# Kernel optimization log

Measured on AMD Instinct MI355X. Metric: run time of the kernel, lower is better.

## Reference

```python
import jax, jax.numpy as jnp
import numpy as np

B, T, D = 2, 2048, 1024
NUM_HEAD = 8
HEAD_DIM = D // NUM_HEAD
CLIP = 2  # _RELATIVE_POS_CLIP


def setup_inputs() -> dict:
    key = jax.random.key(0)
    ks = jax.random.split(key, 12)
    s = 0.02
    return {
        "query": jax.random.normal(ks[0], (B, T, D), jnp.float32),
        "keys": jax.random.normal(ks[1], (B, T, D), jnp.float32),
        "values": jax.random.normal(ks[2], (B, T, D), jnp.float32),
        "Wq": jax.random.normal(ks[3], (D, D), jnp.float32) * s,
        "bq": jnp.zeros((D,), jnp.float32),
        "Wk": jax.random.normal(ks[4], (D, D), jnp.float32) * s,
        "bk": jnp.zeros((D,), jnp.float32),
        "Wv": jax.random.normal(ks[5], (D, D), jnp.float32) * s,
        "bv": jnp.zeros((D,), jnp.float32),
        "Wo": jax.random.normal(ks[6], (D, D), jnp.float32) * s,
        "bo": jnp.zeros((D,), jnp.float32),
        "relpos_table": jax.random.normal(ks[7], (2 * CLIP + 1, D), jnp.float32) * s,
    }


def reference(query, keys, values, Wq, bq, Wk, bk, Wv, bv, Wo, bo, relpos_table):
    Bq, T2, _ = query.shape
    T1 = keys.shape[1]
    # QKV projections (torch Linear: y = x @ W.T + b)
    tq = query @ Wq.T + bq                      # (B, T2, D)
    tk = keys @ Wk.T + bk                       # (B, T1, D)
    tv = values @ Wv.T + bv                     # (B, T1, D)

    # relative-position logits: relpos_embed[i,j] = table[clip(j-i)+CLIP]
    # faithful math via (B,T2,5) dots + gather instead of (T2,T1,D) broadcast
    relpos = jnp.clip(jnp.arange(T1)[None, :] - jnp.arange(T2)[:, None],
                      -CLIP, CLIP) + CLIP        # (T2, T1) int
    proj = tq @ relpos_table.T                   # (B, T2, 2*CLIP+1)
    relpos_logits = proj[:, jnp.arange(T2)[:, None], relpos]  # (B, T2, T1)

    # split heads
    q = tq.reshape(Bq, T2, NUM_HEAD, HEAD_DIM).transpose(0, 2, 1, 3)
    k = tk.reshape(Bq, T1, NUM_HEAD, HEAD_DIM).transpose(0, 2, 1, 3)
    v = tv.reshape(Bq, T1, NUM_HEAD, HEAD_DIM).transpose(0, 2, 1, 3)

    logits = jnp.einsum("bhqd,bhkd->bhqk", q, k)
    logits = (logits + relpos_logits[:, None]) / jnp.sqrt(
        jnp.asarray(HEAD_DIM, logits.dtype))    # scaling after bias, as in nmtlab
    weights = jax.nn.softmax(logits, axis=-1)   # (B, H, T2, T1)
    ctx = jnp.einsum("bhqk,bhkd->bhqd", weights, v)
    ctx = ctx.transpose(0, 2, 1, 3).reshape(Bq, T2, NUM_HEAD * HEAD_DIM)
    out = ctx @ Wo.T + bo                        # (B, T2, D)
    return out, weights
```

## Files before the change

### kernel.cpp

```cpp
#include <hip/hip_runtime.h>
#include <hip/hip_bf16.h>
#include <cmath>

#define Bsz 2
#define Tsz 2048
#define Dsz 1024
#define Hn  8
#define DH  128
#define SCALE 0.08838834764831845f

typedef __attribute__((ext_vector_type(8))) short short8;
typedef __attribute__((ext_vector_type(4))) short short4v;
typedef __attribute__((ext_vector_type(4))) float f32x4;
typedef __hip_bfloat16 bf16;

#define LDK 136

__device__ __forceinline__ float bf2f(unsigned short u) {
    return __uint_as_float(((unsigned)u) << 16);
}
__device__ __forceinline__ unsigned short f2bf(float f) {
    bf16 h = __float2bfloat16(f);
    return *(unsigned short*)&h;
}
__device__ __forceinline__ short8 pack8(float4 a, float4 b) {
    short8 o;
    o[0] = (short)f2bf(a.x); o[1] = (short)f2bf(a.y);
    o[2] = (short)f2bf(a.z); o[3] = (short)f2bf(a.w);
    o[4] = (short)f2bf(b.x); o[5] = (short)f2bf(b.y);
    o[6] = (short)f2bf(b.z); o[7] = (short)f2bf(b.w);
    return o;
}

__device__ __forceinline__ void gload16(const bf16* g, bf16* l) {
    __builtin_amdgcn_global_load_lds(
        (const __attribute__((address_space(1))) void*)g,
        (__attribute__((address_space(3))) void*)l, 16, 0, 0);
}

struct CvtJob { const float* s; bf16* d; int n; };
struct CvtArgs { CvtJob j[4]; };

__global__ __launch_bounds__(256) void cvt_k(CvtArgs a) {
    CvtJob job = a.j[blockIdx.y];
    int idx = (blockIdx.x * 256 + threadIdx.x) * 8;
    const int stride = gridDim.x * 256 * 8;
    for (; idx < job.n; idx += stride) {
        float4 f0 = *(const float4*)(job.s + idx);
        float4 f1 = *(const float4*)(job.s + idx + 4);
        *(short8*)(job.d + idx) = pack8(f0, f1);
    }
}

__device__ __forceinline__ void mfma_step32(const bf16* As, const bf16* Bs,
                                            f32x4 acc[4][4],
                                            int wr, int wc, int fr, int g)
{
    short8 af[4], bfv[4];
#pragma unroll
    for (int m = 0; m < 4; ++m)
        af[m] = *(const short8*)(As + (wr * 64 + m * 16 + fr) * 32 + g * 8);
#pragma unroll
    for (int n = 0; n < 4; ++n)
        bfv[n] = *(const short8*)(Bs + (wc * 64 + n * 16 + fr) * 32 + g * 8);
#pragma unroll
    for (int m = 0; m < 4; ++m)
#pragma unroll
        for (int n = 0; n < 4; ++n)
            acc[m][n] = __builtin_amdgcn_mfma_f32_16x16x32_bf16(
                af[m], bfv[n], acc[m][n], 0, 0, 0);
}

struct GemmJob { const float* A; const bf16* B; const float* bias; void* C; int mode; };
struct GemmArgs { GemmJob j[3]; };

__global__ __launch_bounds__(256, 3) void gemm_qkv_k(GemmArgs args)
{
    __shared__ __align__(16) bf16 As[128 * 32];
    __shared__ __align__(16) bf16 Bs[128 * 32];
    const int bid = blockIdx.x;
    const int wid = (bid & 7) * 96 + (bid >> 3);
    const GemmJob job = args.j[wid >> 8];
    const int t = wid & 255;
    const int row0 = (t >> 3) * 128;
    const int col0 = (t & 7) * 128;
    const int tid = threadIdx.x;
    const int lane = tid & 63;
    const int w = tid >> 6, wr = w >> 1, wc = w & 1;
    const int fr = lane & 15, g = lane >> 4;

    const int srow = lane >> 2, scol = (lane & 3) * 8;
    const float* Ag0 = job.A + (size_t)(row0 + w * 32 + srow) * Dsz + scol;
    const float* Ag1 = Ag0 + 16 * Dsz;
    const bf16*  Bg  = job.B + (size_t)(col0 + w * 32 + srow) * Dsz + scol;
    const int lofs = __builtin_amdgcn_readfirstlane(w * 1024);
    bf16* Bsw = Bs + lofs;
    bf16* Aw0 = As + lofs + lane * 8;
    bf16* Aw1 = Aw0 + 16 * 32;

    f32x4 acc[4][4];
    const f32x4 vz = {0.f, 0.f, 0.f, 0.f};
#pragma unroll
    for (int m = 0; m < 4; ++m)
#pragma unroll
        for (int n = 0; n < 4; ++n) acc[m][n] = vz;

    float4 fa0 = *(const float4*)(Ag0);
    float4 fa1 = *(const float4*)(Ag0 + 4);
    float4 fa2 = *(const float4*)(Ag1);
    float4 fa3 = *(const float4*)(Ag1 + 4);

#pragma unroll 1
    for (int k0 = 0; k0 < Dsz; k0 += 32) {
        __syncthreads();
        *(short8*)Aw0 = pack8(fa0, fa1);
        *(short8*)Aw1 = pack8(fa2, fa3);
        gload16(Bg + k0, Bsw);
        gload16(Bg + 16 * Dsz + k0, Bsw + 16 * 32);
        __syncthreads();
        if (k0 + 32 < Dsz) {
            fa0 = *(const float4*)(Ag0 + k0 + 32);
            fa1 = *(const float4*)(Ag0 + k0 + 36);
            fa2 = *(const float4*)(Ag1 + k0 + 32);
            fa3 = *(const float4*)(Ag1 + k0 + 36);
        }
        mfma_step32(As, Bs, acc, wr, wc, fr, g);
    }

    if (job.mode == 2) {
        bf16* vtp = (bf16*)job.C;
#pragma unroll
        for (int m = 0; m < 4; ++m) {
            const int gi0 = row0 + wr * 64 + m * 16 + g * 4;
            const int bidx = gi0 >> 11, jj = gi0 & 2047;
#pragma unroll
            for (int n = 0; n < 4; ++n) {
                const int gj = col0 + wc * 64 + n * 16 + fr;
                const float bv = job.bias[gj];
                short4v pk;
#pragma unroll
                for (int r = 0; r < 4; ++r)
                    pk[r] = (short)f2bf(acc[m][n][r] + bv);
                const size_t zrow = ((size_t)bidx * 8 + (gj >> 7)) * 128 + (gj & 127);
                *(short4v*)(vtp + zrow * Tsz + jj) = pk;
            }
        }
    } else {
#pragma unroll
        for (int m = 0; m < 4; ++m) {
#pragma unroll
            for (int r = 0; r < 4; ++r) {
                const int gi = row0 + wr * 64 + m * 16 + g * 4 + r;
#pragma unroll
                for (int n = 0; n < 4; ++n) {
                    const int gj = col0 + wc * 64 + n * 16 + fr;
                    float x = acc[m][n][r] + job.bias[gj];
                    ((bf16*)job.C)[(size_t)gi * Dsz + gj] = __float2bfloat16(x);
                }
            }
        }
    }
}

__global__ __launch_bounds__(256) void relproj_k(
    const bf16* __restrict__ tq, const float* __restrict__ table,
    float* __restrict__ proj)
{
    const int row  = blockIdx.x * 4 + (threadIdx.x >> 6);
    const int lane = threadIdx.x & 63;
    const bf16* qrow = tq + (size_t)row * Dsz;
    float acc[5] = {0.f, 0.f, 0.f, 0.f, 0.f};
#pragma unroll
    for (int t = 0; t < 4; ++t) {
        const int d = t * 256 + lane * 4;
        short4v q4 = *(const short4v*)(qrow + d);
        float qv[4];
#pragma unroll
        for (int q = 0; q < 4; ++q) qv[q] = bf2f((unsigned short)q4[q]);
#pragma unroll
        for (int c = 0; c < 5; ++c) {
            float4 t4 = *(const float4*)(table + c * Dsz + d);
            acc[c] = fmaf(qv[0], t4.x, acc[c]);
            acc[c] = fmaf(qv[1], t4.y, acc[c]);
            acc[c] = fmaf(qv[2], t4.z, acc[c]);
            acc[c] = fmaf(qv[3], t4.w, acc[c]);
        }
    }
#pragma unroll
    for (int c = 0; c < 5; ++c)
        for (int off = 32; off > 0; off >>= 1)
            acc[c] += __shfl_xor(acc[c], off);
    if (lane == 0) {
#pragma unroll
        for (int c = 0; c < 5; ++c)
            proj[(size_t)row * 8 + c] = acc[c];
    }
}

__global__ __launch_bounds__(512) void flash_pv_k(
    const bf16* __restrict__ tq, const bf16* __restrict__ tk,
    const bf16* __restrict__ vt, const float* __restrict__ proj,
    float* __restrict__ invs_g, bf16* __restrict__ ctx)
{
    __shared__ __align__(16) bf16 Ks[128 * LDK];
    __shared__ __align__(16) bf16 Vs[128 * LDK];
    __shared__ __align__(16) bf16 Ps[128 * 128];
    __shared__ float proj_s[5 * 132];

    const int tid = threadIdx.x;
    const int bid = blockIdx.x;
    const int wid = (bid & 7) * 32 + (bid >> 3);
    const int qt = wid & 15, z = wid >> 4;
    const int b = z >> 3, h = z & 7;
    const int i0 = qt * 128;
    const int lane = tid & 63, w = tid >> 6;
    const int fr = lane & 15, g = lane >> 4;
    const int il = w * 16 + fr;
    const int srow = tid >> 2, scb = (tid & 3) * 32;

    if (tid < 128) {
        const float* pr = proj + (size_t)(b * Tsz + i0 + tid) * 8;
#pragma unroll
        for (int c = 0; c < 5; ++c) proj_s[c * 132 + tid] = pr[c];
    }

    const bf16* qrow = tq + (size_t)(b * Tsz + i0 + il) * Dsz + h * DH + g * 8;
    short8 qf[4];
#pragma unroll
    for (int ks = 0; ks < 4; ++ks)
        qf[ks] = *(const short8*)(qrow + ks * 32);

    f32x4 accp[8];
    const f32x4 vz = {0.f, 0.f, 0.f, 0.f};
#pragma unroll
    for (int n = 0; n < 8; ++n) accp[n] = vz;
    float rs = 0.f;

    const bf16* kg = tk + (size_t)(b * Tsz + srow) * Dsz + h * DH + scb;
    const bf16* vg = vt + ((size_t)z * DH + srow) * Tsz + scb;
    short8 kv[4], vv[4];
#pragma unroll
    for (int q = 0; q < 4; ++q) kv[q] = *(const short8*)(kg + q * 8);
#pragma unroll
    for (int q = 0; q < 4; ++q) vv[q] = *(const short8*)(vg + q * 8);

#pragma unroll 1
    for (int kt = 0; kt < Tsz / 128; ++kt) {
        __syncthreads();
#pragma unroll
        for (int q = 0; q < 4; ++q) *(short8*)(Ks + srow * LDK + scb + q * 8) = kv[q];
#pragma unroll
        for (int q = 0; q < 4; ++q) *(short8*)(Vs + srow * LDK + scb + q * 8) = vv[q];
        __syncthreads();

        if (kt + 1 < Tsz / 128) {
            const bf16* kn = kg + (size_t)(kt + 1) * 128 * Dsz;
            const bf16* vn = vg + (kt + 1) * 128;
#pragma unroll
            for (int q = 0; q < 4; ++q) kv[q] = *(const short8*)(kn + q * 8);
#pragma unroll
            for (int q = 0; q < 4; ++q) vv[q] = *(const short8*)(vn + q * 8);
        }

        f32x4 as_[8];
#pragma unroll
        for (int m = 0; m < 8; ++m) as_[m] = vz;
        __builtin_amdgcn_s_setprio(1);
#pragma unroll
        for (int ks = 0; ks < 4; ++ks) {
            short8 kf[8];
#pragma unroll
            for (int mj = 0; mj < 8; ++mj)
                kf[mj] = *(const short8*)(Ks + (mj * 16 + fr) * LDK + ks * 32 + g * 8);
#pragma unroll
            for (int mj = 0; mj < 8; ++mj)
                as_[mj] = __builtin_amdgcn_mfma_f32_16x16x32_bf16(
                    kf[mj], qf[ks], as_[mj], 0, 0, 0);
        }
        __builtin_amdgcn_s_setprio(0);

        const int dt = kt - qt;
        const int pbase = il * 256;
        const int swz = (il & 7) << 4;
        if (dt <= -2 || dt >= 2) {
            const float bias = proj_s[((dt >= 2) ? 4 : 0) * 132 + il];
#pragma unroll
            for (int mj = 0; mj < 8; ++mj) {
                const int jl0 = mj * 16 + g * 4;
                short4v pk;
#pragma unroll
                for (int r = 0; r < 4; ++r) {
                    float p = __expf((as_[mj][r] + bias) * SCALE);
                    rs += p;
                    pk[r] = (short)f2bf(p);
                }
                *(short4v*)((char*)Ps + ((pbase + jl0 * 2) ^ swz)) = pk;
            }
        } else {
#pragma unroll
            for (int mj = 0; mj < 8; ++mj) {
                const int jl0 = mj * 16 + g * 4;
                short4v pk;
#pragma unroll
                for (int r = 0; r < 4; ++r) {
                    int dd = (jl0 + r + dt * 128) - il;
                    dd = dd < -2 ? -2 : (dd > 2 ? 2 : dd);
                    const float bias = proj_s[(dd + 2) * 132 + il];
                    float p = __expf((as_[mj][r] + bias) * SCALE);
                    rs += p;
                    pk[r] = (short)f2bf(p);
                }
                *(short4v*)((char*)Ps + ((pbase + jl0 * 2) ^ swz)) = pk;
            }
        }

        __builtin_amdgcn_s_setprio(1);
#pragma unroll
        for (int ks = 0; ks < 4; ++ks) {
            short8 pf = *(const short8*)((char*)Ps +
                            ((pbase + (ks * 32 + g * 8) * 2) ^ swz));
            short8 vf[8];
#pragma unroll
            for (int n2 = 0; n2 < 8; ++n2)
                vf[n2] = *(const short8*)(Vs + (n2 * 16 + fr) * LDK + ks * 32 + g * 8);
#pragma unroll
            for (int n2 = 0; n2 < 8; ++n2)
                accp[n2] = __builtin_amdgcn_mfma_f32_16x16x32_bf16(
                    pf, vf[n2], accp[n2], 0, 0, 0);
        }
        __builtin_amdgcn_s_setprio(0);
    }

    rs += __shfl_xor(rs, 16);
    rs += __shfl_xor(rs, 32);
    const float iv = 1.0f / rs;
    if (g == 0)
        invs_g[(size_t)z * Tsz + i0 + il] = iv;

    float ivr[4];
#pragma unroll
    for (int r = 0; r < 4; ++r) ivr[r] = __shfl(iv, g * 4 + r);

    bf16* cp = ctx + (size_t)(b * Tsz + i0 + w * 16) * Dsz + h * DH;
#pragma unroll
    for (int r = 0; r < 4; ++r) {
        const int irow = g * 4 + r;
#pragma unroll
        for (int n2 = 0; n2 < 8; ++n2)
            cp[(size_t)irow * Dsz + n2 * 16 + fr] = __float2bfloat16(accp[n2][r] * ivr[r]);
    }
}

__global__ __launch_bounds__(512) void wo_k(
    const bf16* __restrict__ tq, const bf16* __restrict__ tk,
    const float* __restrict__ proj, const float* __restrict__ invs_g,
    float* __restrict__ Wt,
    const bf16* __restrict__ ctx, const bf16* __restrict__ Wob,
    const float* __restrict__ bo, float* __restrict__ out)
{
    __shared__ __align__(16) bf16 As[256 * 32];
    __shared__ __align__(16) bf16 Bs[256 * 32];
    __shared__ float proj_s[5 * 264];
    __shared__ float inv_s[256];

    const int tid = threadIdx.x;
    const int lane = tid & 63, w = tid >> 6;
    const int fr = lane & 15, g = lane >> 4;
    const int wj = w & 3, wi = w >> 2;
    const int srow = lane >> 2, scol = (lane & 3) * 8;
    const int lofs = __builtin_amdgcn_readfirstlane(w * 1024);
    bf16* Asw = As + lofs;
    bf16* Bsw = Bs + lofs;
    const f32x4 vz = {0.f, 0.f, 0.f, 0.f};
    const int bid = blockIdx.x;

    if (bid >= 64) {
        const int b0 = bid - 64;
        const int wid = (b0 & 7) * 128 + (b0 >> 3);
        const int z = wid >> 6;
        const int t = wid & 63;
        const int row0 = (t >> 3) * 256;
        const int col0 = (t & 7) * 256;
        const int b = z >> 3, h = z & 7;

        if (tid < 256) {
            const float* pr = proj + (size_t)(b * Tsz + row0 + tid) * 8;
#pragma unroll
            for (int c = 0; c < 5; ++c) proj_s[c * 264 + tid] = pr[c];
        } else {
            inv_s[tid - 256] = invs_g[(size_t)z * Tsz + row0 + (tid - 256)];
        }

        const bf16* Ag = tk + (size_t)(b * Tsz + col0 + w * 32 + srow) * Dsz + h * DH + scol;
        const bf16* Bg = tq + (size_t)(b * Tsz + row0 + w * 32 + srow) * Dsz + h * DH + scol;

        f32x4 acc[4][8];
#pragma unroll
        for (int m = 0; m < 4; ++m)
#pragma unroll
            for (int n = 0; n < 8; ++n) acc[m][n] = vz;

#pragma unroll 1
        for (int k0 = 0; k0 < DH; k0 += 32) {
            __syncthreads();
            gload16(Ag + k0, Asw);
            gload16(Ag + 16 * Dsz + k0, Asw + 16 * 32);
            gload16(Bg + k0, Bsw);
            gload16(Bg + 16 * Dsz + k0, Bsw + 16 * 32);
            __syncthreads();
            short8 af[4], bfv[8];
#pragma unroll
            for (int jf = 0; jf < 4; ++jf)
                af[jf] = *(const short8*)(As + (wj * 64 + jf * 16 + fr) * 32 + g * 8);
#pragma unroll
            for (int ii = 0; ii < 8; ++ii)
                bfv[ii] = *(const short8*)(Bs + (wi * 128 + ii * 16 + fr) * 32 + g * 8);
#pragma unroll
            for (int jf = 0; jf < 4; ++jf)
#pragma unroll
                for (int ii = 0; ii < 8; ++ii)
                    acc[jf][ii] = __builtin_amdgcn_mfma_f32_16x16x32_bf16(
                        af[jf], bfv[ii], acc[jf][ii], 0, 0, 0);
        }

        float* C = Wt + (size_t)z * Tsz * Tsz;
        const int dmin = col0 - (row0 + 255);
        const int dmax = (col0 + 255) - row0;
        if (dmin >= 2 || dmax <= -2) {
            const int c = (dmin >= 2) ? 4 : 0;
#pragma unroll
            for (int ii = 0; ii < 8; ++ii) {
                const int il = wi * 128 + ii * 16 + fr;
                const int gi = row0 + il;
                const float iv = inv_s[il];
                const float bias = proj_s[c * 264 + il];
#pragma unroll
                for (int jf = 0; jf < 4; ++jf) {
                    const int jb = col0 + wj * 64 + jf * 16 + g * 4;
                    f32x4 o;
#pragma unroll
                    for (int r = 0; r < 4; ++r)
                        o[r] = __expf((acc[jf][ii][r] + bias) * SCALE) * iv;
                    __builtin_nontemporal_store(o, (f32x4*)(C + (size_t)gi * Tsz + jb));
                }
            }
        } else {
#pragma unroll
            for (int ii = 0; ii < 8; ++ii) {
                const int il = wi * 128 + ii * 16 + fr;
                const int gi = row0 + il;
                const float iv = inv_s[il];
#pragma unroll
                for (int jf = 0; jf < 4; ++jf) {
                    const int jb = col0 + wj * 64 + jf * 16 + g * 4;
                    f32x4 o;
#pragma unroll
                    for (int r = 0; r < 4; ++r) {
                        int rel = (jb + r) - gi;
                        rel = rel < -2 ? -2 : (rel > 2 ? 2 : rel);
                        const float bias = proj_s[(rel + 2) * 264 + il];
                        o[r] = __expf((acc[jf][ii][r] + bias) * SCALE) * iv;
                    }
                    __builtin_nontemporal_store(o, (f32x4*)(C + (size_t)gi * Tsz + jb));
                }
            }
        }
    } else {
        const int row0 = (bid >> 2) * 256;
        const int col0 = (bid & 3) * 256;
        const bf16* Ag = ctx + (size_t)(row0 + w * 32 + srow) * Dsz + scol;
        const bf16* Bg = Wob + (size_t)(col0 + w * 32 + srow) * Dsz + scol;

        f32x4 acc2[8][4];
#pragma unroll
        for (int m = 0; m < 8; ++m)
#pragma unroll
            for (int n = 0; n < 4; ++n) acc2[m][n] = vz;

#pragma unroll 1
        for (int k0 = 0; k0 < Dsz; k0 += 32) {
            __syncthreads();
            gload16(Ag + k0, Asw);
            gload16(Ag + 16 * Dsz + k0, Asw + 16 * 32);
            gload16(Bg + k0, Bsw);
            gload16(Bg + 16 * Dsz + k0, Bsw + 16 * 32);
            __syncthreads();
            short8 af[8], bfv[4];
#pragma unroll
            for (int ii = 0; ii < 8; ++ii)
                af[ii] = *(const short8*)(As + (wi * 128 + ii * 16 + fr) * 32 + g * 8);
#pragma unroll
            for (int jc = 0; jc < 4; ++jc)
                bfv[jc] = *(const short8*)(Bs + (wj * 64 + jc * 16 + fr) * 32 + g * 8);
#pragma unroll
            for (int ii = 0; ii < 8; ++ii)
#pragma unroll
                for (int jc = 0; jc < 4; ++jc)
                    acc2[ii][jc] = __builtin_amdgcn_mfma_f32_16x16x32_bf16(
                        af[ii], bfv[jc], acc2[ii][jc], 0, 0, 0);
        }

#pragma unroll
        for (int ii = 0; ii < 8; ++ii) {
#pragma unroll
            for (int r = 0; r < 4; ++r) {
                const int gi = row0 + wi * 128 + ii * 16 + g * 4 + r;
#pragma unroll
                for (int jc = 0; jc < 4; ++jc) {
                    const int gj = col0 + wj * 64 + jc * 16 + fr;
                    out[(size_t)gi * Dsz + gj] = acc2[ii][jc][r] + bo[gj];
                }
            }
        }
    }
}

extern "C" void kernel_launch(void* const* d_in, const int* in_sizes, int n_in,
                              void* d_out, int out_size, void* d_ws, size_t ws_size,
                              hipStream_t stream)
{
    const float* query  = (const float*)d_in[0];
    const float* keys   = (const float*)d_in[1];
    const float* values = (const float*)d_in[2];
    const float* Wq = (const float*)d_in[3];
    const float* bq = (const float*)d_in[4];
    const float* Wk = (const float*)d_in[5];
    const float* bk = (const float*)d_in[6];
    const float* Wv = (const float*)d_in[7];
    const float* bv = (const float*)d_in[8];
    const float* Wo = (const float*)d_in[9];
    const float* bo = (const float*)d_in[10];
    const float* table = (const float*)d_in[11];

    float* out     = (float*)d_out;
    float* weights = out + (size_t)Bsz * Tsz * Dsz;

    char* wp = (char*)d_ws;
    bf16* tq  = (bf16*)(wp);
    bf16* tk  = (bf16*)(wp + 8  * 1024 * 1024);
    bf16* vt  = (bf16*)(wp + 16 * 1024 * 1024);
    bf16* ctx = (bf16*)(wp + 24 * 1024 * 1024);
    bf16* Wqb = (bf16*)(wp + 32 * 1024 * 1024);
    bf16* Wkb = (bf16*)(wp + 34 * 1024 * 1024);
    bf16* Wvb = (bf16*)(wp + 36 * 1024 * 1024);
    bf16* Wob = (bf16*)(wp + 38 * 1024 * 1024);
    float* proj   = (float*)(wp + 40 * 1024 * 1024);
    float* invs_g = (float*)(wp + 41 * 1024 * 1024);

    const dim3 blk(256);

    CvtArgs ca;
    ca.j[0] = { Wq, Wqb, Dsz * Dsz };
    ca.j[1] = { Wk, Wkb, Dsz * Dsz };
    ca.j[2] = { Wv, Wvb, Dsz * Dsz };
    ca.j[3] = { Wo, Wob, Dsz * Dsz };
    cvt_k<<<dim3(128, 4), blk, 0, stream>>>(ca);

    GemmArgs ga;
    ga.j[0] = { query,  Wqb, bq, tq, 1 };
    ga.j[1] = { keys,   Wkb, bk, tk, 1 };
    ga.j[2] = { values, Wvb, bv, vt, 2 };
    gemm_qkv_k<<<dim3(768), blk, 0, stream>>>(ga);

    relproj_k<<<dim3(Bsz * Tsz / 4), blk, 0, stream>>>(tq, table, proj);

    flash_pv_k<<<dim3(256), dim3(512), 0, stream>>>(
        tq, tk, vt, proj, invs_g, ctx);

    wo_k<<<dim3(64 + 1024), dim3(512), 0, stream>>>(
        tq, tk, proj, invs_g, weights, ctx, Wob, bo, out);
}
```

Before: 193.0 us.

## Switch flash PV kernel to 32x32x16 MFMA with register-resident P

Rewrites the attention inner loop to use 32x32x16 bf16 MFMAs, with warps split into 4 query groups × 2 key halves. The probabilities stay in registers and are repacked via lane shuffles as the PV operand, which removes the shared-memory P buffer and its round trip. Partial row sums and accumulators from the two key halves are combined through shared scratch at the end. This trades extra shuffles and a final reduction for fewer LDS writes and reads and larger MFMA tiles.

```diff
diff --git a/kernel.cpp b/kernel.cpp
--- a/kernel.cpp
+++ b/kernel.cpp
@@ -12,6 +12,8 @@
 typedef __attribute__((ext_vector_type(8))) short short8;
 typedef __attribute__((ext_vector_type(4))) short short4v;
 typedef __attribute__((ext_vector_type(4))) float f32x4;
+typedef __attribute__((ext_vector_type(16))) float f32x16;
+typedef __attribute__((ext_vector_type(4))) unsigned int uint4v;
 typedef __hip_bfloat16 bf16;
 
 #define LDK 136
@@ -22,6 +24,9 @@
 __device__ __forceinline__ unsigned short f2bf(float f) {
     bf16 h = __float2bfloat16(f);
     return *(unsigned short*)&h;
+}
+__device__ __forceinline__ unsigned pk2(float lo, float hi) {
+    return (unsigned)f2bf(lo) | ((unsigned)f2bf(hi) << 16);
 }
 __device__ __forceinline__ short8 pack8(float4 a, float4 b) {
     short8 o;
@@ -202,10 +207,12 @@
     const bf16* __restrict__ vt, const float* __restrict__ proj,
     float* __restrict__ invs_g, bf16* __restrict__ ctx)
 {
-    __shared__ __align__(16) bf16 Ks[128 * LDK];
-    __shared__ __align__(16) bf16 Vs[128 * LDK];
-    __shared__ __align__(16) bf16 Ps[128 * 128];
+    __shared__ __align__(16) char smem[2 * 128 * LDK * 2];
     __shared__ float proj_s[5 * 132];
+    __shared__ float sums_l[8 * 32];
+    bf16* Ks = (bf16*)smem;
+    bf16* Vs = Ks + 128 * LDK;
+    float* scratch = (float*)smem;
 
     const int tid = threadIdx.x;
     const int bid = blockIdx.x;
@@ -214,8 +221,9 @@
     const int b = z >> 3, h = z & 7;
     const int i0 = qt * 128;
     const int lane = tid & 63, w = tid >> 6;
-    const int fr = lane & 15, g = lane >> 4;
-    const int il = w * 16 + fr;
+    const int il = lane & 31, hi = lane >> 5;
+    const int ig = w & 3, jh = w >> 2;
+    const int i_local = ig * 32 + il;
     const int srow = tid >> 2, scb = (tid & 3) * 32;
 
     if (tid < 128) {
@@ -224,16 +232,17 @@
         for (int c = 0; c < 5; ++c) proj_s[c * 132 + tid] = pr[c];
     }
 
-    const bf16* qrow = tq + (size_t)(b * Tsz + i0 + il) * Dsz + h * DH + g * 8;
-    short8 qf[4];
-#pragma unroll
-    for (int ks = 0; ks < 4; ++ks)
-        qf[ks] = *(const short8*)(qrow + ks * 32);
-
-    f32x4 accp[8];
-    const f32x4 vz = {0.f, 0.f, 0.f, 0.f};
-#pragma unroll
-    for (int n = 0; n < 8; ++n) accp[n] = vz;
+    const bf16* qrow = tq + (size_t)(b * Tsz + i0 + i_local) * Dsz + h * DH + hi * 8;
+    short8 qf[8];
+#pragma unroll
+    for (int kc = 0; kc < 8; ++kc)
+        qf[kc] = *(const short8*)(qrow + kc * 16);
+
+    f32x16 accp[4];
+#pragma unroll
+    for (int d4 = 0; d4 < 4; ++d4)
+#pragma unroll
+        for (int e = 0; e < 16; ++e) accp[d4][e] = 0.f;
     float rs = 0.f;
 
     const bf16* kg = tk + (size_t)(b * Tsz + srow) * Dsz + h * DH + scb;
@@ -262,92 +271,105 @@
             for (int q = 0; q < 4; ++q) vv[q] = *(const short8*)(vn + q * 8);
         }
 
-        f32x4 as_[8];
-#pragma unroll
-        for (int m = 0; m < 8; ++m) as_[m] = vz;
+        f32x16 as_[2];
+#pragma unroll
+        for (int jf = 0; jf < 2; ++jf)
+#pragma unroll
+            for (int e = 0; e < 16; ++e) as_[jf][e] = 0.f;
         __builtin_amdgcn_s_setprio(1);
 #pragma unroll
-        for (int ks = 0; ks < 4; ++ks) {
-            short8 kf[8];
-#pragma unroll
-            for (int mj = 0; mj < 8; ++mj)
-                kf[mj] = *(const short8*)(Ks + (mj * 16 + fr) * LDK + ks * 32 + g * 8);
-#pragma unroll
-            for (int mj = 0; mj < 8; ++mj)
-                as_[mj] = __builtin_amdgcn_mfma_f32_16x16x32_bf16(
-                    kf[mj], qf[ks], as_[mj], 0, 0, 0);
+        for (int kc = 0; kc < 8; ++kc) {
+            short8 kf0 = *(const short8*)(Ks + (jh * 64 + il) * LDK + kc * 16 + hi * 8);
+            short8 kf1 = *(const short8*)(Ks + (jh * 64 + 32 + il) * LDK + kc * 16 + hi * 8);
+            as_[0] = __builtin_amdgcn_mfma_f32_32x32x16_bf16(kf0, qf[kc], as_[0], 0, 0, 0);
+            as_[1] = __builtin_amdgcn_mfma_f32_32x32x16_bf16(kf1, qf[kc], as_[1], 0, 0, 0);
         }
         __builtin_amdgcn_s_setprio(0);
 
         const int dt = kt - qt;
-        const int pbase = il * 256;
-        const int swz = (il & 7) << 4;
         if (dt <= -2 || dt >= 2) {
-            const float bias = proj_s[((dt >= 2) ? 4 : 0) * 132 + il];
-#pragma unroll
-            for (int mj = 0; mj < 8; ++mj) {
-                const int jl0 = mj * 16 + g * 4;
-                short4v pk;
-#pragma unroll
-                for (int r = 0; r < 4; ++r) {
-                    float p = __expf((as_[mj][r] + bias) * SCALE);
+            const float bias = proj_s[((dt >= 2) ? 4 : 0) * 132 + i_local];
+#pragma unroll
+            for (int jf = 0; jf < 2; ++jf)
+#pragma unroll
+                for (int e = 0; e < 16; ++e) {
+                    float p = __expf((as_[jf][e] + bias) * SCALE);
                     rs += p;
-                    pk[r] = (short)f2bf(p);
+                    as_[jf][e] = p;
                 }
-                *(short4v*)((char*)Ps + ((pbase + jl0 * 2) ^ swz)) = pk;
-            }
         } else {
 #pragma unroll
-            for (int mj = 0; mj < 8; ++mj) {
-                const int jl0 = mj * 16 + g * 4;
-                short4v pk;
-#pragma unroll
-                for (int r = 0; r < 4; ++r) {
-                    int dd = (jl0 + r + dt * 128) - il;
+            for (int jf = 0; jf < 2; ++jf)
+#pragma unroll
+                for (int e = 0; e < 16; ++e) {
+                    const int jloc = jh * 64 + jf * 32 + (e & 3) + 8 * (e >> 2) + 4 * hi;
+                    int dd = (jloc + dt * 128) - i_local;
                     dd = dd < -2 ? -2 : (dd > 2 ? 2 : dd);
-                    const float bias = proj_s[(dd + 2) * 132 + il];
-                    float p = __expf((as_[mj][r] + bias) * SCALE);
+                    const float bias = proj_s[(dd + 2) * 132 + i_local];
+                    float p = __expf((as_[jf][e] + bias) * SCALE);
                     rs += p;
-                    pk[r] = (short)f2bf(p);
+                    as_[jf][e] = p;
                 }
-                *(short4v*)((char*)Ps + ((pbase + jl0 * 2) ^ swz)) = pk;
-            }
-        }
+        }
+
+        unsigned pw[2][8];
+#pragma unroll
+        for (int jf = 0; jf < 2; ++jf)
+#pragma unroll
+            for (int q = 0; q < 8; ++q)
+                pw[jf][q] = pk2(as_[jf][2 * q], as_[jf][2 * q + 1]);
 
         __builtin_amdgcn_s_setprio(1);
 #pragma unroll
-        for (int ks = 0; ks < 4; ++ks) {
-            short8 pf = *(const short8*)((char*)Ps +
-                            ((pbase + (ks * 32 + g * 8) * 2) ^ swz));
-            short8 vf[8];
-#pragma unroll
-            for (int n2 = 0; n2 < 8; ++n2)
-                vf[n2] = *(const short8*)(Vs + (n2 * 16 + fr) * LDK + ks * 32 + g * 8);
-#pragma unroll
-            for (int n2 = 0; n2 < 8; ++n2)
-                accp[n2] = __builtin_amdgcn_mfma_f32_16x16x32_bf16(
-                    pf, vf[n2], accp[n2], 0, 0, 0);
+        for (int chunk = 0; chunk < 4; ++chunk) {
+            const int jf = chunk >> 1;
+            const int c2 = (chunk & 1) * 2;
+            unsigned W0a = pw[jf][c2 * 2],       W0b = pw[jf][c2 * 2 + 1];
+            unsigned W1a = pw[jf][(c2 + 1) * 2], W1b = pw[jf][(c2 + 1) * 2 + 1];
+            unsigned X0a = __shfl_xor((int)W0a, 32), X0b = __shfl_xor((int)W0b, 32);
+            unsigned X1a = __shfl_xor((int)W1a, 32), X1b = __shfl_xor((int)W1b, 32);
+            uint4v u;
+            u[0] = hi == 0 ? W0a : X1a;
+            u[1] = hi == 0 ? W0b : X1b;
+            u[2] = hi == 0 ? X0a : W1a;
+            u[3] = hi == 0 ? X0b : W1b;
+            short8 pb = *(short8*)&u;
+            const int jcol = jh * 64 + chunk * 16 + hi * 8;
+#pragma unroll
+            for (int d4 = 0; d4 < 4; ++d4) {
+                short8 vtf = *(const short8*)(Vs + (d4 * 32 + il) * LDK + jcol);
+                accp[d4] = __builtin_amdgcn_mfma_f32_32x32x16_bf16(vtf, pb, accp[d4], 0, 0, 0);
+            }
         }
         __builtin_amdgcn_s_setprio(0);
     }
 
-    rs += __shfl_xor(rs, 16);
     rs += __shfl_xor(rs, 32);
-    const float iv = 1.0f / rs;
-    if (g == 0)
-        invs_g[(size_t)z * Tsz + i0 + il] = iv;
-
-    float ivr[4];
-#pragma unroll
-    for (int r = 0; r < 4; ++r) ivr[r] = __shfl(iv, g * 4 + r);
-
-    bf16* cp = ctx + (size_t)(b * Tsz + i0 + w * 16) * Dsz + h * DH;
-#pragma unroll
-    for (int r = 0; r < 4; ++r) {
-        const int irow = g * 4 + r;
-#pragma unroll
-        for (int n2 = 0; n2 < 8; ++n2)
-            cp[(size_t)irow * Dsz + n2 * 16 + fr] = __float2bfloat16(accp[n2][r] * ivr[r]);
+    if (lane < 32) sums_l[w * 32 + il] = rs;
+    __syncthreads();
+    const float total = sums_l[ig * 32 + il] + sums_l[(ig + 4) * 32 + il];
+    const float iv = 1.0f / total;
+    if (jh == 0 && hi == 0)
+        invs_g[(size_t)z * Tsz + i0 + i_local] = iv;
+
+    if (jh == 1) {
+#pragma unroll
+        for (int d4 = 0; d4 < 4; ++d4)
+#pragma unroll
+            for (int e = 0; e < 16; ++e)
+                scratch[((ig * 4 + d4) * 16 + e) * 64 + lane] = accp[d4][e];
+    }
+    __syncthreads();
+    if (jh == 0) {
+        bf16* cp = ctx + (size_t)(b * Tsz + i0 + i_local) * Dsz + h * DH;
+#pragma unroll
+        for (int d4 = 0; d4 < 4; ++d4)
+#pragma unroll
+            for (int e = 0; e < 16; ++e) {
+                float v = accp[d4][e] + scratch[((ig * 4 + d4) * 16 + e) * 64 + lane];
+                const int d = d4 * 32 + (e & 3) + 8 * (e >> 2) + 4 * hi;
+                cp[d] = __float2bfloat16(v * iv);
+            }
     }
 }
 
```

Result: faster. 187.3 us (median of 2 runs) (-2.9%).
